# Performance work log

Hardware: AMD Instinct MI355X
Metric: run time of the kernel (lower is better)

## Reference

```python
import jax, jax.numpy as jnp
import numpy as np
import math

D = 768
H = 12
DFF = 3072
HD = D // H


def _layernorm(x, g, b, eps=1e-5):
    mu = jnp.mean(x, axis=-1, keepdims=True)
    var = jnp.var(x, axis=-1, keepdims=True)
    return (x - mu) * jax.lax.rsqrt(var + eps) * g + b


def setup_inputs() -> dict:
    key = jax.random.key(0)
    ks = jax.random.split(key, 12)
    B, S = 2, 4096
    s = 1.0 / math.sqrt(D)
    sf = 1.0 / math.sqrt(DFF)
    return {
        "x": jax.random.normal(ks[0], (B, S, D), jnp.float32),
        "attention_mask": jnp.ones((B, S), jnp.int32),
        "ln1_g": jnp.ones((D,), jnp.float32),
        "ln1_b": jnp.zeros((D,), jnp.float32),
        "ln2_g": jnp.ones((D,), jnp.float32),
        "ln2_b": jnp.zeros((D,), jnp.float32),
        "Wq": jax.random.normal(ks[1], (D, D), jnp.float32) * s,
        "bq": jnp.zeros((D,), jnp.float32),
        "Wk": jax.random.normal(ks[2], (D, D), jnp.float32) * s,
        "bk": jnp.zeros((D,), jnp.float32),
        "Wv": jax.random.normal(ks[3], (D, D), jnp.float32) * s,
        "bv": jnp.zeros((D,), jnp.float32),
        "Wo": jax.random.normal(ks[4], (D, D), jnp.float32) * s,
        "bo": jnp.zeros((D,), jnp.float32),
        "W1": jax.random.normal(ks[5], (D, DFF), jnp.float32) * s,
        "b1": jnp.zeros((DFF,), jnp.float32),
        "W2": jax.random.normal(ks[6], (DFF, D), jnp.float32) * sf,
        "b2": jnp.zeros((D,), jnp.float32),
    }


def _block(x, attention_mask, ln1_g, ln1_b, ln2_g, ln2_b,
           Wq, bq, Wk, bk, Wv, bv, Wo, bo, W1, b1, W2, b2):
    B, S, _ = x.shape
    h = _layernorm(x, ln1_g, ln1_b)
    q = (h @ Wq + bq).reshape(B, S, H, HD)
    k = (h @ Wk + bk).reshape(B, S, H, HD)
    v = (h @ Wv + bv).reshape(B, S, H, HD)
    # scores: [B, H, S, S]
    dots = jnp.einsum('bqhd,bkhd->bhqk', q, k) / math.sqrt(HD)
    causal = jnp.tril(jnp.ones((S, S), bool))  # True = keep
    keep = causal[None, None] & (attention_mask != 0)[:, None, None, :]
    dots = jnp.where(keep, dots, -jnp.inf)
    probs = jax.nn.softmax(dots, axis=-1)
    ctx = jnp.einsum('bhqk,bkhd->bqhd', probs, v).reshape(B, S, D)
    sa = ctx @ Wo + bo  # dropout = identity (eval)
    x = x + sa
    h2 = _layernorm(x, ln2_g, ln2_b)
    ff = jax.nn.relu(h2 @ W1 + b1) @ W2 + b2
    return x + ff


def reference(x, attention_mask, ln1_g, ln1_b, ln2_g, ln2_b,
              Wq, bq, Wk, bk, Wv, bv, Wo, bo, W1, b1, W2, b2):
    return _block(x, attention_mask, ln1_g, ln1_b, ln2_g, ln2_b,
                  Wq, bq, Wk, bk, Wv, bv, Wo, bo, W1, b1, W2, b2)
```

## Files before the change

kernel.cpp:

```cpp
#include <hip/hip_runtime.h>
#include <hip/hip_bf16.h>
#include <math.h>

#define S_LEN 4096
#define DMODEL 768
#define NHEAD 12
#define HDIM 64
#define DFF_ 3072
#define MROWS 8192

typedef __bf16 bf16;
typedef __bf16 bf16x4 __attribute__((ext_vector_type(4)));
typedef __bf16 bf16x8 __attribute__((ext_vector_type(8)));
typedef float f32x4 __attribute__((ext_vector_type(4)));
typedef short s16x4 __attribute__((ext_vector_type(4)));

union F4 { float4 v; float f[4]; };
union U2 { bf16 h[2]; unsigned u; };
union U8 { unsigned u[4]; bf16x8 v; };

#if __has_builtin(__builtin_amdgcn_mfma_f32_16x16x16bf16_1k)
typedef s16x4 mf16_t;
#define MFMA16(a, b, c) __builtin_amdgcn_mfma_f32_16x16x16bf16_1k((a), (b), (c), 0, 0, 0)
#define HAVE_MFMA16 1
#elif __has_builtin(__builtin_amdgcn_mfma_f32_16x16x16_bf16)
typedef bf16x4 mf16_t;
#define MFMA16(a, b, c) __builtin_amdgcn_mfma_f32_16x16x16_bf16((a), (b), (c), 0, 0, 0)
#define HAVE_MFMA16 1
#else
#define HAVE_MFMA16 0
#endif

#if HAVE_MFMA16
union U4 { unsigned u[2]; mf16_t v; };
#endif

__device__ __forceinline__ void gld_lds16(void* lds, const void* g) {
    __builtin_amdgcn_global_load_lds(
        (const __attribute__((address_space(1))) unsigned int*)g,
        (__attribute__((address_space(3))) unsigned int*)lds, 16, 0, 0);
}

template<typename OUT>
__global__ __launch_bounds__(256) void ln_kernel(const float* __restrict__ x,
                                                 const float* __restrict__ g,
                                                 const float* __restrict__ bta,
                                                 OUT* __restrict__ out,
                                                 float* __restrict__ zb) {
    const int row = blockIdx.x;
    const int t = threadIdx.x;
    if (zb && row == 0 && t < 192)
        ((float4*)zb)[t] = make_float4(0.f, 0.f, 0.f, 0.f);
    const float* xr = x + (size_t)row * DMODEL;
    float v0 = xr[t], v1 = xr[t + 256], v2 = xr[t + 512];
    float s = v0 + v1 + v2;
    float ss = v0 * v0 + v1 * v1 + v2 * v2;
    for (int o = 32; o > 0; o >>= 1) {
        s += __shfl_down(s, o, 64);
        ss += __shfl_down(ss, o, 64);
    }
    __shared__ float sm[4], sm2[4];
    const int w = t >> 6, lane = t & 63;
    if (lane == 0) { sm[w] = s; sm2[w] = ss; }
    __syncthreads();
    s = sm[0] + sm[1] + sm[2] + sm[3];
    ss = sm2[0] + sm2[1] + sm2[2] + sm2[3];
    const float mu = s * (1.0f / DMODEL);
    const float var = ss * (1.0f / DMODEL) - mu * mu;
    const float rs = rsqrtf(var + 1e-5f);
    OUT* orow = out + (size_t)row * DMODEL;
    orow[t]       = (OUT)((v0 - mu) * rs * g[t]       + bta[t]);
    orow[t + 256] = (OUT)((v1 - mu) * rs * g[t + 256] + bta[t + 256]);
    orow[t + 512] = (OUT)((v2 - mu) * rs * g[t + 512] + bta[t + 512]);
}

__global__ __launch_bounds__(256) void wtrans_all_kernel(
    const float* __restrict__ Wq, const float* __restrict__ Wk,
    const float* __restrict__ Wv, const float* __restrict__ Wo,
    const float* __restrict__ W1, const float* __restrict__ W2,
    bf16* __restrict__ Wqt, bf16* __restrict__ Wkt, bf16* __restrict__ Wvt,
    bf16* __restrict__ Wot, bf16* __restrict__ W1t, bf16* __restrict__ W2t) {
    int t = blockIdx.x;
    const float* W; bf16* Wt; int K, N;
    if      (t < 144)  { W = Wq; Wt = Wqt; K = 768;  N = 768;  }
    else if (t < 288)  { W = Wk; Wt = Wkt; K = 768;  N = 768;  t -= 144; }
    else if (t < 432)  { W = Wv; Wt = Wvt; K = 768;  N = 768;  t -= 288; }
    else if (t < 576)  { W = Wo; Wt = Wot; K = 768;  N = 768;  t -= 432; }
    else if (t < 1152) { W = W1; Wt = W1t; K = 768;  N = 3072; t -= 576; }
    else               { W = W2; Wt = W2t; K = 3072; N = 768;  t -= 1152; }
    const int nx = N >> 6;
    const int n0 = (t % nx) * 64, k0 = (t / nx) * 64;

    __shared__ float tile[64][65];
    const int tid = threadIdx.x;
    const int lr = tid >> 4, lc = (tid & 15) << 2;
#pragma unroll
    for (int i = 0; i < 4; ++i) {
        const int r = lr + i * 16;
        F4 w; w.v = *(const float4*)&W[(size_t)(k0 + r) * N + n0 + lc];
#pragma unroll
        for (int j = 0; j < 4; ++j) tile[r][lc + j] = w.f[j];
    }
    __syncthreads();
#pragma unroll
    for (int i = 0; i < 4; ++i) {
        const int n = lr + i * 16;
        bf16x4 o;
#pragma unroll
        for (int j = 0; j < 4; ++j) o[j] = (bf16)tile[lc + j][n];
        *(bf16x4*)&Wt[(size_t)(n0 + n) * K + k0 + lc] = o;
    }
}

template<int MT, bool RELU, bool RES, bool OUT_BF16>
__global__ __launch_bounds__(256) void mgemm_kernel(
    const bf16* __restrict__ A,
    const bf16* __restrict__ Wt0, const float* __restrict__ bias0, void* __restrict__ C0,
    const bf16* __restrict__ Wt1, const float* __restrict__ bias1, void* __restrict__ C1,
    const bf16* __restrict__ Wt2, const float* __restrict__ bias2, void* __restrict__ C2,
    const float* __restrict__ R, int M, int N, int K, int Kloop,
    int koff0, int koff1, int koff2,
    float sc0, float sc1, float sc2) {
    const bf16* Wt = Wt0; const float* bias = bias0; void* C = C0; float sc = sc0; int koff = koff0;
    if (blockIdx.z == 1) { Wt = Wt1; bias = bias1; C = C1; sc = sc1; koff = koff1; }
    if (blockIdx.z == 2) { Wt = Wt2; bias = bias2; C = C2; sc = sc2; koff = koff2; }

    constexpr int NI = (MT == 128) ? 4 : 2;
    __shared__ bf16 As[2][MT * 32];
    __shared__ bf16 Bs[2][128 * 32];

    const int tid = threadIdx.x;
    const int wave = tid >> 6, lane = tid & 63;
    const int row0 = blockIdx.y * MT, col0 = blockIdx.x * 128;
    const int wr = (MT == 128) ? (wave >> 1) * 64 : 0;
    const int wc = (MT == 128) ? (wave & 1) * 64 : wave * 32;
    const int mrow = lane & 15, kq = (lane >> 4) * 8;

    const int st_row = (lane >> 2);
    const int st_off = (lane & 3) * 16;

    f32x4 acc[4][NI] = {};

    const char* Ab = (const char*)(A + (size_t)row0 * K + koff);
    const char* Bb = (const char*)(Wt + (size_t)col0 * K + koff);
    const size_t strideA = (size_t)K * 2;

    for (int k0 = 0; k0 < Kloop; k0 += 64) {
#pragma unroll
        for (int s = 0; s < 2; ++s) {
            const int kk = k0 + s * 32;
            if (MT == 128) {
#pragma unroll
                for (int issue = 0; issue < 2; ++issue) {
                    const int r = wave * 32 + issue * 16 + st_row;
                    gld_lds16((char*)As[s] + (wave * 32 + issue * 16) * 64,
                              Ab + (size_t)r * strideA + kk * 2 + st_off);
                }
            } else {
                const int r = wave * 16 + st_row;
                gld_lds16((char*)As[s] + (wave * 16) * 64,
                          Ab + (size_t)r * strideA + kk * 2 + st_off);
            }
#pragma unroll
            for (int issue = 0; issue < 2; ++issue) {
                const int r = wave * 32 + issue * 16 + st_row;
                gld_lds16((char*)Bs[s] + (wave * 32 + issue * 16) * 64,
                          Bb + (size_t)r * strideA + kk * 2 + st_off);
            }
        }
        __syncthreads();
#pragma unroll
        for (int s = 0; s < 2; ++s) {
            bf16x8 af[4], bfr[NI];
#pragma unroll
            for (int mi = 0; mi < 4; ++mi)
                af[mi] = *(const bf16x8*)&As[s][(wr + mi * 16 + mrow) * 32 + kq];
#pragma unroll
            for (int ni = 0; ni < NI; ++ni)
                bfr[ni] = *(const bf16x8*)&Bs[s][(wc + ni * 16 + mrow) * 32 + kq];
#pragma unroll
            for (int mi = 0; mi < 4; ++mi)
#pragma unroll
                for (int ni = 0; ni < NI; ++ni)
                    acc[mi][ni] = __builtin_amdgcn_mfma_f32_16x16x32_bf16(
                        af[mi], bfr[ni], acc[mi][ni], 0, 0, 0);
        }
        __syncthreads();
    }

    const int quad = lane >> 4;
    float bv[NI];
#pragma unroll
    for (int ni = 0; ni < NI; ++ni) bv[ni] = bias[col0 + wc + ni * 16 + mrow];
#pragma unroll
    for (int mi = 0; mi < 4; ++mi) {
#pragma unroll
        for (int r = 0; r < 4; ++r) {
            const int row = row0 + wr + mi * 16 + quad * 4 + r;
#pragma unroll
            for (int ni = 0; ni < NI; ++ni) {
                const int col = col0 + wc + ni * 16 + mrow;
                float v = acc[mi][ni][r] + bv[ni];
                if (RES) v += R[(size_t)row * N + col];
                v *= sc;
                if (RELU) v = fmaxf(v, 0.0f);
                if (OUT_BF16) ((bf16*)C)[(size_t)row * N + col] = (bf16)v;
                else          ((float*)C)[(size_t)row * N + col] = v;
            }
        }
    }
}

__global__ __launch_bounds__(256) void ff2_combine_kernel(
    const bf16* __restrict__ p0, const bf16* __restrict__ p1,
    const float* __restrict__ b2, const float* __restrict__ x1,
    float* __restrict__ out) {
    const int i = (blockIdx.x * 256 + threadIdx.x) * 4;
    bf16x4 a = *(const bf16x4*)(p0 + i);
    bf16x4 b = *(const bf16x4*)(p1 + i);
    F4 xr; xr.v = *(const float4*)(x1 + i);
    const int col = i % DMODEL;
    F4 o;
#pragma unroll
    for (int j = 0; j < 4; ++j)
        o.f[j] = (float)a[j] + (float)b[j] + b2[col + j] + xr.f[j];
    *(float4*)(out + i) = o.v;
}

__global__ __launch_bounds__(256) void mattn_kernel(
    const bf16* __restrict__ Q, const bf16* __restrict__ K,
    const bf16* __restrict__ V, const int* __restrict__ amask,
    bf16* __restrict__ O) {
    const int qt = 63 - blockIdx.x;
    const int h = blockIdx.y, b = blockIdx.z;

    __shared__ bf16 Ks[2][64][68];
    __shared__ bf16 Vt[2][64][68];
    __shared__ float mk[2][64];
    __shared__ int flagv[2];

    const int tid = threadIdx.x;
    const int wave = tid >> 6, lane = tid & 63;
    const int l = lane & 15, quad = lane >> 4;
#if !HAVE_MFMA16
    const int qh = quad >> 1;
    const int srcA = (quad & 1) * 32 + l;
    const int srcB = srcA + 16;
#endif
    const float NEG_INF = -__builtin_huge_valf();

    const int kr = tid >> 2, ks = (tid & 3) * 16;
    const int vk0 = (tid & 31) * 2, vds = (tid >> 5) * 8;

    const bf16* Kbase = K + (size_t)b * S_LEN * DMODEL + h * HDIM;
    const bf16* Vbase = V + (size_t)b * S_LEN * DMODEL + h * HDIM;

#if HAVE_MFMA16
    U4 onesf;
    onesf.u[0] = 0x3F803F80u; onesf.u[1] = 0x3F803F80u;
#endif

    const bf16* Qb = Q + (size_t)(b * S_LEN + qt * 64 + wave * 16 + l) * DMODEL + h * HDIM;
    const bf16x8 qf0 = *(const bf16x8*)(Qb + quad * 8);
    const bf16x8 qf1 = *(const bf16x8*)(Qb + 32 + quad * 8);

    float m_run = NEG_INF;
#if !HAVE_MFMA16
    float l_run = 0.0f;
#endif
    f32x4 acc[4] = {};
#if HAVE_MFMA16
    f32x4 acc_l = {};
#endif

    bf16x8 kp0, kp1, vp0, vp1;
    int mv = 1;
    {
        const bf16* kg = Kbase + (size_t)kr * DMODEL + ks;
        kp0 = *(const bf16x8*)kg;
        kp1 = *(const bf16x8*)(kg + 8);
        const bf16* vg = Vbase + (size_t)vk0 * DMODEL + vds;
        vp0 = *(const bf16x8*)vg;
        vp1 = *(const bf16x8*)(vg + DMODEL);
        if (wave == 0) mv = amask[b * S_LEN + lane];
        *(bf16x8*)&Ks[0][kr][ks]     = kp0;
        *(bf16x8*)&Ks[0][kr][ks + 8] = kp1;
#pragma unroll
        for (int i = 0; i < 8; ++i) {
            U2 w; w.h[0] = vp0[i]; w.h[1] = vp1[i];
            *(unsigned*)&Vt[0][vds + i][vk0] = w.u;
        }
        if (wave == 0) {
            mk[0][lane] = mv ? 0.0f : NEG_INF;
            unsigned long long bal = __ballot(mv != 0);
            if (lane == 0) flagv[0] = (bal == ~0ULL);
        }
    }
    __syncthreads();
    int buf = 0;

    for (int kt = 0; kt <= qt; ++kt) {
        const bool more = (kt < qt);
        if (more) {
            const bf16* kg = Kbase + (size_t)((kt + 1) * 64 + kr) * DMODEL + ks;
            kp0 = *(const bf16x8*)kg;
            kp1 = *(const bf16x8*)(kg + 8);
            const bf16* vg = Vbase + (size_t)((kt + 1) * 64 + vk0) * DMODEL + vds;
            vp0 = *(const bf16x8*)vg;
            vp1 = *(const bf16x8*)(vg + DMODEL);
            if (wave == 0) mv = amask[b * S_LEN + (kt + 1) * 64 + lane];
        }

        const int allv = flagv[buf];
        f32x4 sreg[4] = {};
        __builtin_amdgcn_s_setprio(1);
#pragma unroll
        for (int mi = 0; mi < 4; ++mi) {
            bf16x8 kf0 = *(const bf16x8*)&Ks[buf][mi * 16 + l][quad * 8];
            bf16x8 kf1 = *(const bf16x8*)&Ks[buf][mi * 16 + l][32 + quad * 8];
            sreg[mi] = __builtin_amdgcn_mfma_f32_16x16x32_bf16(kf0, qf0, sreg[mi], 0, 0, 0);
            sreg[mi] = __builtin_amdgcn_mfma_f32_16x16x32_bf16(kf1, qf1, sreg[mi], 0, 0, 0);
        }
        __builtin_amdgcn_s_setprio(0);
        if (!allv) {
#pragma unroll
            for (int mi = 0; mi < 4; ++mi) {
                F4 m4; m4.v = *(const float4*)&mk[buf][mi * 16 + quad * 4];
#pragma unroll
                for (int r = 0; r < 4; ++r) sreg[mi][r] += m4.f[r];
            }
        }
        if (kt == qt) {
#pragma unroll
            for (int mi = 0; mi < 4; ++mi)
#pragma unroll
                for (int r = 0; r < 4; ++r)
                    if (mi * 16 + quad * 4 + r > wave * 16 + l)
                        sreg[mi][r] = NEG_INF;
        }

        float mloc = sreg[0][0];
#pragma unroll
        for (int mi = 0; mi < 4; ++mi)
#pragma unroll
            for (int r = 0; r < 4; ++r) mloc = fmaxf(mloc, sreg[mi][r]);
        mloc = fmaxf(mloc, __shfl_xor(mloc, 16, 64));
        mloc = fmaxf(mloc, __shfl_xor(mloc, 32, 64));
        if (__any(mloc > m_run + 8.0f)) {
            const float mn = fmaxf(m_run, mloc);
            const float alpha = __builtin_amdgcn_exp2f(m_run - mn);
            m_run = mn;
#pragma unroll
            for (int mi = 0; mi < 4; ++mi)
#pragma unroll
                for (int r = 0; r < 4; ++r) acc[mi][r] *= alpha;
#if HAVE_MFMA16
#pragma unroll
            for (int r = 0; r < 4; ++r) acc_l[r] *= alpha;
#else
            l_run *= alpha;
#endif
        }
#pragma unroll
        for (int mi = 0; mi < 4; ++mi)
#pragma unroll
            for (int r = 0; r < 4; ++r)
                sreg[mi][r] = __builtin_amdgcn_exp2f(sreg[mi][r] - m_run);
#if !HAVE_MFMA16
        float ls = 0.0f;
#pragma unroll
        for (int mi = 0; mi < 4; ++mi)
#pragma unroll
            for (int r = 0; r < 4; ++r) ls += sreg[mi][r];
        ls += __shfl_xor(ls, 16, 64);
        ls += __shfl_xor(ls, 32, 64);
        l_run += ls;
#endif

        unsigned pk[4][2];
#pragma unroll
        for (int mi = 0; mi < 4; ++mi) {
            U2 w0; w0.h[0] = (bf16)sreg[mi][0]; w0.h[1] = (bf16)sreg[mi][1];
            U2 w1; w1.h[0] = (bf16)sreg[mi][2]; w1.h[1] = (bf16)sreg[mi][3];
            pk[mi][0] = w0.u; pk[mi][1] = w1.u;
        }

#if HAVE_MFMA16
        __builtin_amdgcn_s_setprio(1);
#pragma unroll
        for (int mi = 0; mi < 4; ++mi) {
            U4 pb; pb.u[0] = pk[mi][0]; pb.u[1] = pk[mi][1];
#pragma unroll
            for (int di = 0; di < 4; ++di) {
                mf16_t va = *(const mf16_t*)&Vt[buf][di * 16 + l][mi * 16 + quad * 4];
                acc[di] = MFMA16(va, pb.v, acc[di]);
            }
            acc_l = MFMA16(onesf.v, pb.v, acc_l);
        }
        __builtin_amdgcn_s_setprio(0);
#else
        bf16x8 pfrag[2];
#pragma unroll
        for (int kc = 0; kc < 2; ++kc) {
            U8 u;
#pragma unroll
            for (int t = 0; t < 2; ++t) {
                const unsigned a0 = (unsigned)__shfl((int)pk[2 * kc][t],     srcA, 64);
                const unsigned b0 = (unsigned)__shfl((int)pk[2 * kc + 1][t], srcA, 64);
                u.u[t] = qh ? b0 : a0;
                const unsigned a1 = (unsigned)__shfl((int)pk[2 * kc][t],     srcB, 64);
                const unsigned b1 = (unsigned)__shfl((int)pk[2 * kc + 1][t], srcB, 64);
                u.u[2 + t] = qh ? b1 : a1;
            }
            pfrag[kc] = u.v;
        }
#pragma unroll
        for (int mi = 0; mi < 4; ++mi) {
            bf16x8 vf0 = *(const bf16x8*)&Vt[buf][mi * 16 + l][quad * 8];
            bf16x8 vf1 = *(const bf16x8*)&Vt[buf][mi * 16 + l][32 + quad * 8];
            acc[mi] = __builtin_amdgcn_mfma_f32_16x16x32_bf16(vf0, pfrag[0], acc[mi], 0, 0, 0);
            acc[mi] = __builtin_amdgcn_mfma_f32_16x16x32_bf16(vf1, pfrag[1], acc[mi], 0, 0, 0);
        }
#endif

        if (more) {
            const int nb = buf ^ 1;
            *(bf16x8*)&Ks[nb][kr][ks]     = kp0;
            *(bf16x8*)&Ks[nb][kr][ks + 8] = kp1;
#pragma unroll
            for (int i = 0; i < 8; ++i) {
                U2 w; w.h[0] = vp0[i]; w.h[1] = vp1[i];
                *(unsigned*)&Vt[nb][vds + i][vk0] = w.u;
            }
            if (wave == 0) {
                mk[nb][lane] = mv ? 0.0f : NEG_INF;
                unsigned long long bal = __ballot(mv != 0);
                if (lane == 0) flagv[nb] = (bal == ~0ULL);
            }
        }
        __syncthreads();
        buf ^= 1;
    }

#if HAVE_MFMA16
    const float l_fin = __shfl(acc_l[0], l, 64);
#else
    const float l_fin = l_run;
#endif
    const float rinv = 1.0f / l_fin;
    bf16 (*Os)[68] = (bf16 (*)[68])(&Ks[0][0][0]);
#pragma unroll
    for (int mi = 0; mi < 4; ++mi) {
        U2 w0; w0.h[0] = (bf16)(acc[mi][0] * rinv); w0.h[1] = (bf16)(acc[mi][1] * rinv);
        U2 w1; w1.h[0] = (bf16)(acc[mi][2] * rinv); w1.h[1] = (bf16)(acc[mi][3] * rinv);
        *(unsigned*)&Os[wave * 16 + l][mi * 16 + quad * 4]     = w0.u;
        *(unsigned*)&Os[wave * 16 + l][mi * 16 + quad * 4 + 2] = w1.u;
    }
    __syncthreads();
    {
        const int orow = tid >> 2, oseg = (tid & 3) * 16;
        bf16* Og = O + (size_t)(b * S_LEN + qt * 64 + orow) * DMODEL + h * HDIM + oseg;
        *(bf16x8*)Og       = *(const bf16x8*)&Os[orow][oseg];
        *(bf16x8*)(Og + 8) = *(const bf16x8*)&Os[orow][oseg + 8];
    }
}

extern "C" void kernel_launch(void* const* d_in, const int* in_sizes, int n_in,
                              void* d_out, int out_size, void* d_ws, size_t ws_size,
                              hipStream_t stream) {
    const float* x     = (const float*)d_in[0];
    const int*   amask = (const int*)  d_in[1];
    const float* ln1_g = (const float*)d_in[2];
    const float* ln1_b = (const float*)d_in[3];
    const float* ln2_g = (const float*)d_in[4];
    const float* ln2_b = (const float*)d_in[5];
    const float* Wq = (const float*)d_in[6];  const float* bq = (const float*)d_in[7];
    const float* Wk = (const float*)d_in[8];  const float* bk = (const float*)d_in[9];
    const float* Wv = (const float*)d_in[10]; const float* bv = (const float*)d_in[11];
    const float* Wo = (const float*)d_in[12]; const float* bo = (const float*)d_in[13];
    const float* W1 = (const float*)d_in[14]; const float* b1 = (const float*)d_in[15];
    const float* W2 = (const float*)d_in[16]; const float* b2 = (const float*)d_in[17];
    float* out = (float*)d_out;

    char* ws = (char*)d_ws;
    const size_t WSML = (size_t)DMODEL * DMODEL * 2;
    const size_t WBIG = (size_t)DMODEL * DFF_ * 2;
    bf16* Wqt = (bf16*)(ws + 0 * WSML);
    bf16* Wkt = (bf16*)(ws + 1 * WSML);
    bf16* Wvt = (bf16*)(ws + 2 * WSML);
    bf16* Wot = (bf16*)(ws + 3 * WSML);
    bf16* W1t = (bf16*)(ws + 4 * WSML);
    bf16* W2t = (bf16*)(ws + 4 * WSML + WBIG);
    char* act = ws + 4 * WSML + 2 * WBIG;

    const size_t HB = (size_t)MROWS * DMODEL * 2;
    const size_t FB = (size_t)MROWS * DMODEL * 4;
    bf16*  h    = (bf16*)(act);
    bf16*  qb   = (bf16*)(act + HB);
    bf16*  kb   = (bf16*)(act + 2 * HB);
    bf16*  vb   = (bf16*)(act + 3 * HB);
    bf16*  ctx  = h;
    float* x1   = (float*)(act + 4 * HB);
    bf16*  f    = (bf16*)(act + 4 * HB + FB);
    bf16*  h2   = h;
    bf16*  p0   = qb;
    bf16*  p1   = kb;
    float* zbias = (float*)vb;

    const float SCL = 0.125f * 1.44269504089f;

    wtrans_all_kernel<<<1728, 256, 0, stream>>>(Wq, Wk, Wv, Wo, W1, W2,
                                                Wqt, Wkt, Wvt, Wot, W1t, W2t);

    ln_kernel<bf16><<<MROWS, 256, 0, stream>>>(x, ln1_g, ln1_b, h, nullptr);
    mgemm_kernel<128, false, false, true><<<dim3(DMODEL / 128, MROWS / 128, 3), 256, 0, stream>>>(
        h, Wqt, bq, qb, Wkt, bk, kb, Wvt, bv, vb, nullptr,
        MROWS, DMODEL, DMODEL, DMODEL, 0, 0, 0, SCL, 1.0f, 1.0f);
    mattn_kernel<<<dim3(64, NHEAD, 2), 256, 0, stream>>>(qb, kb, vb, amask, ctx);
    mgemm_kernel<64, false, true, false><<<dim3(DMODEL / 128, MROWS / 64, 1), 256, 0, stream>>>(
        ctx, Wot, bo, x1, Wot, bo, x1, Wot, bo, x1, x,
        MROWS, DMODEL, DMODEL, DMODEL, 0, 0, 0, 1.0f, 1.0f, 1.0f);
    ln_kernel<bf16><<<MROWS, 256, 0, stream>>>(x1, ln2_g, ln2_b, h2, zbias);
    mgemm_kernel<128, true, false, true><<<dim3(DFF_ / 128, MROWS / 128, 1), 256, 0, stream>>>(
        h2, W1t, b1, f, W1t, b1, f, W1t, b1, f, nullptr,
        MROWS, DFF_, DMODEL, DMODEL, 0, 0, 0, 1.0f, 1.0f, 1.0f);
    mgemm_kernel<128, false, false, true><<<dim3(DMODEL / 128, MROWS / 128, 2), 256, 0, stream>>>(
        f, W2t, zbias, p0, W2t, zbias, p1, W2t, zbias, p1, nullptr,
        MROWS, DMODEL, DFF_, DFF_ / 2, 0, DFF_ / 2, 0, 1.0f, 1.0f, 1.0f);
    ff2_combine_kernel<<<(MROWS * DMODEL) / 1024, 256, 0, stream>>>(p0, p1, b2, x1, out);
}
```

Before: 518.5 us.

## Pair causal query tiles per block and load V via async LDS with transpose reads

The attention kernel now processes two query tiles per block (tile 63-bx and tile bx), so every block does the same amount of causal work, and the grid shrinks to half. V tiles are copied straight from global memory into LDS with global_load_lds, skipping the register round trip and the scalar transpose stores. The PV fragments are then read with ds_read_b64_tr_b16. The PV MFMA operands are swapped so the softmax rescale is applied per row through shuffles. This trades fewer, longer blocks (less occupancy and parallelism slack) for balanced load and a cheaper V staging path.

```diff
diff --git a/kernel.cpp b/kernel.cpp
--- a/kernel.cpp
+++ b/kernel.cpp
@@ -14,31 +14,31 @@
 typedef __bf16 bf16x8 __attribute__((ext_vector_type(8)));
 typedef float f32x4 __attribute__((ext_vector_type(4)));
 typedef short s16x4 __attribute__((ext_vector_type(4)));
+typedef s16x4 frag4;
 
 union F4 { float4 v; float f[4]; };
-union U2 { bf16 h[2]; unsigned u; };
-union U8 { unsigned u[4]; bf16x8 v; };
-
-#if __has_builtin(__builtin_amdgcn_mfma_f32_16x16x16bf16_1k)
-typedef s16x4 mf16_t;
-#define MFMA16(a, b, c) __builtin_amdgcn_mfma_f32_16x16x16bf16_1k((a), (b), (c), 0, 0, 0)
-#define HAVE_MFMA16 1
-#elif __has_builtin(__builtin_amdgcn_mfma_f32_16x16x16_bf16)
-typedef bf16x4 mf16_t;
-#define MFMA16(a, b, c) __builtin_amdgcn_mfma_f32_16x16x16_bf16((a), (b), (c), 0, 0, 0)
-#define HAVE_MFMA16 1
-#else
-#define HAVE_MFMA16 0
-#endif
-
-#if HAVE_MFMA16
-union U4 { unsigned u[2]; mf16_t v; };
-#endif
 
 __device__ __forceinline__ void gld_lds16(void* lds, const void* g) {
     __builtin_amdgcn_global_load_lds(
         (const __attribute__((address_space(1))) unsigned int*)g,
         (__attribute__((address_space(3))) unsigned int*)lds, 16, 0, 0);
+}
+
+__device__ __forceinline__ unsigned lds_off(const void* p) {
+    return (unsigned)(size_t)(const __attribute__((address_space(3))) char*)p;
+}
+
+__device__ __forceinline__ f32x4 mfma16(frag4 a, frag4 b, f32x4 c) {
+#if __has_builtin(__builtin_amdgcn_mfma_f32_16x16x16bf16_1k)
+    return __builtin_amdgcn_mfma_f32_16x16x16bf16_1k(a, b, c, 0, 0, 0);
+#else
+    union { frag4 s; bf16x4 h; } ua, ub; ua.s = a; ub.s = b;
+    bf16x8 a8 = {ua.h[0], ua.h[1], ua.h[2], ua.h[3],
+                 (bf16)0.f, (bf16)0.f, (bf16)0.f, (bf16)0.f};
+    bf16x8 b8 = {ub.h[0], ub.h[1], ub.h[2], ub.h[3],
+                 (bf16)0.f, (bf16)0.f, (bf16)0.f, (bf16)0.f};
+    return __builtin_amdgcn_mfma_f32_16x16x32_bf16(a8, b8, c, 0, 0, 0);
+#endif
 }
 
 template<typename OUT>
@@ -231,237 +231,201 @@
     const bf16* __restrict__ Q, const bf16* __restrict__ K,
     const bf16* __restrict__ V, const int* __restrict__ amask,
     bf16* __restrict__ O) {
-    const int qt = 63 - blockIdx.x;
-    const int h = blockIdx.y, b = blockIdx.z;
+    const int bx = blockIdx.x, h = blockIdx.y, b = blockIdx.z;
 
     __shared__ bf16 Ks[2][64][68];
-    __shared__ bf16 Vt[2][64][68];
+    __shared__ bf16 Vs[2][4096];
     __shared__ float mk[2][64];
     __shared__ int flagv[2];
 
     const int tid = threadIdx.x;
     const int wave = tid >> 6, lane = tid & 63;
     const int l = lane & 15, quad = lane >> 4;
-#if !HAVE_MFMA16
-    const int qh = quad >> 1;
-    const int srcA = (quad & 1) * 32 + l;
-    const int srcB = srcA + 16;
-#endif
     const float NEG_INF = -__builtin_huge_valf();
 
     const int kr = tid >> 2, ks = (tid & 3) * 16;
-    const int vk0 = (tid & 31) * 2, vds = (tid >> 5) * 8;
 
     const bf16* Kbase = K + (size_t)b * S_LEN * DMODEL + h * HDIM;
     const bf16* Vbase = V + (size_t)b * S_LEN * DMODEL + h * HDIM;
 
-#if HAVE_MFMA16
-    U4 onesf;
-    onesf.u[0] = 0x3F803F80u; onesf.u[1] = 0x3F803F80u;
-#endif
-
-    const bf16* Qb = Q + (size_t)(b * S_LEN + qt * 64 + wave * 16 + l) * DMODEL + h * HDIM;
-    const bf16x8 qf0 = *(const bf16x8*)(Qb + quad * 8);
-    const bf16x8 qf1 = *(const bf16x8*)(Qb + 32 + quad * 8);
-
-    float m_run = NEG_INF;
-#if !HAVE_MFMA16
-    float l_run = 0.0f;
-#endif
-    f32x4 acc[4] = {};
-#if HAVE_MFMA16
-    f32x4 acc_l = {};
-#endif
-
-    bf16x8 kp0, kp1, vp0, vp1;
-    int mv = 1;
+    int voff0, voff1;
     {
-        const bf16* kg = Kbase + (size_t)kr * DMODEL + ks;
-        kp0 = *(const bf16x8*)kg;
-        kp1 = *(const bf16x8*)(kg + 8);
-        const bf16* vg = Vbase + (size_t)vk0 * DMODEL + vds;
-        vp0 = *(const bf16x8*)vg;
-        vp1 = *(const bf16x8*)(vg + DMODEL);
-        if (wave == 0) mv = amask[b * S_LEN + lane];
-        *(bf16x8*)&Ks[0][kr][ks]     = kp0;
-        *(bf16x8*)&Ks[0][kr][ks + 8] = kp1;
-#pragma unroll
-        for (int i = 0; i < 8; ++i) {
-            U2 w; w.h[0] = vp0[i]; w.h[1] = vp1[i];
-            *(unsigned*)&Vt[0][vds + i][vk0] = w.u;
-        }
-        if (wave == 0) {
-            mk[0][lane] = mv ? 0.0f : NEG_INF;
-            unsigned long long bal = __ballot(mv != 0);
-            if (lane == 0) flagv[0] = (bal == ~0ULL);
-        }
-    }
-    __syncthreads();
-    int buf = 0;
-
-    for (int kt = 0; kt <= qt; ++kt) {
-        const bool more = (kt < qt);
-        if (more) {
-            const bf16* kg = Kbase + (size_t)((kt + 1) * 64 + kr) * DMODEL + ks;
+        const int g0 = tid, s0 = g0 >> 5;
+        voff0 = ((s0 >> 2) * 16 + ((g0 >> 1) & 15)) * DMODEL + (s0 & 3) * 16 + (g0 & 1) * 8;
+        const int g1 = 256 + tid, s1 = g1 >> 5;
+        voff1 = ((s1 >> 2) * 16 + ((g1 >> 1) & 15)) * DMODEL + (s1 & 3) * 16 + (g1 & 1) * 8;
+    }
+    const int vdst0 = (wave * 64) * 16;
+    const int vdst1 = (256 + wave * 64) * 16;
+
+    const frag4 onesf = {(short)0x3F80, (short)0x3F80, (short)0x3F80, (short)0x3F80};
+    const unsigned vtr0 = lds_off(&Vs[0][0]) + lane * 8;
+
+#pragma unroll 1
+    for (int pass = 0; pass < 2; ++pass) {
+        const int qt = pass ? bx : (63 - bx);
+
+        const bf16* Qb = Q + (size_t)(b * S_LEN + qt * 64 + wave * 16 + l) * DMODEL + h * HDIM;
+        const bf16x8 qf0 = *(const bf16x8*)(Qb + quad * 8);
+        const bf16x8 qf1 = *(const bf16x8*)(Qb + 32 + quad * 8);
+
+        float m_run = NEG_INF;
+        f32x4 acc[4] = {};
+        f32x4 acc_l = {};
+
+        bf16x8 kp0, kp1;
+        int mv = 1;
+        {
+            const bf16* kg = Kbase + (size_t)kr * DMODEL + ks;
             kp0 = *(const bf16x8*)kg;
             kp1 = *(const bf16x8*)(kg + 8);
-            const bf16* vg = Vbase + (size_t)((kt + 1) * 64 + vk0) * DMODEL + vds;
-            vp0 = *(const bf16x8*)vg;
-            vp1 = *(const bf16x8*)(vg + DMODEL);
-            if (wave == 0) mv = amask[b * S_LEN + (kt + 1) * 64 + lane];
-        }
-
-        const int allv = flagv[buf];
-        f32x4 sreg[4] = {};
-        __builtin_amdgcn_s_setprio(1);
-#pragma unroll
-        for (int mi = 0; mi < 4; ++mi) {
-            bf16x8 kf0 = *(const bf16x8*)&Ks[buf][mi * 16 + l][quad * 8];
-            bf16x8 kf1 = *(const bf16x8*)&Ks[buf][mi * 16 + l][32 + quad * 8];
-            sreg[mi] = __builtin_amdgcn_mfma_f32_16x16x32_bf16(kf0, qf0, sreg[mi], 0, 0, 0);
-            sreg[mi] = __builtin_amdgcn_mfma_f32_16x16x32_bf16(kf1, qf1, sreg[mi], 0, 0, 0);
-        }
-        __builtin_amdgcn_s_setprio(0);
-        if (!allv) {
+            gld_lds16((char*)Vs + vdst0, Vbase + voff0);
+            gld_lds16((char*)Vs + vdst1, Vbase + voff1);
+            if (wave == 0) mv = amask[b * S_LEN + lane];
+        }
+        __syncthreads();
+        {
+            *(bf16x8*)&Ks[0][kr][ks]     = kp0;
+            *(bf16x8*)&Ks[0][kr][ks + 8] = kp1;
+            if (wave == 0) {
+                mk[0][lane] = mv ? 0.0f : NEG_INF;
+                unsigned long long bal = __ballot(mv != 0);
+                if (lane == 0) flagv[0] = (bal == ~0ULL);
+            }
+        }
+        __syncthreads();
+        int buf = 0;
+
+        for (int kt = 0; kt <= qt; ++kt) {
+            const bool more = (kt < qt);
+            if (more) {
+                const bf16* kg = Kbase + (size_t)((kt + 1) * 64 + kr) * DMODEL + ks;
+                kp0 = *(const bf16x8*)kg;
+                kp1 = *(const bf16x8*)(kg + 8);
+                const bf16* vt = Vbase + (size_t)(kt + 1) * 64 * DMODEL;
+                const int nb = buf ^ 1;
+                gld_lds16((char*)Vs + nb * 8192 + vdst0, vt + voff0);
+                gld_lds16((char*)Vs + nb * 8192 + vdst1, vt + voff1);
+                if (wave == 0) mv = amask[b * S_LEN + (kt + 1) * 64 + lane];
+            }
+
+            const int allv = flagv[buf];
+            f32x4 sreg[4] = {};
+            __builtin_amdgcn_s_setprio(1);
 #pragma unroll
             for (int mi = 0; mi < 4; ++mi) {
-                F4 m4; m4.v = *(const float4*)&mk[buf][mi * 16 + quad * 4];
-#pragma unroll
-                for (int r = 0; r < 4; ++r) sreg[mi][r] += m4.f[r];
-            }
-        }
-        if (kt == qt) {
+                bf16x8 kf0 = *(const bf16x8*)&Ks[buf][mi * 16 + l][quad * 8];
+                bf16x8 kf1 = *(const bf16x8*)&Ks[buf][mi * 16 + l][32 + quad * 8];
+                sreg[mi] = __builtin_amdgcn_mfma_f32_16x16x32_bf16(kf0, qf0, sreg[mi], 0, 0, 0);
+                sreg[mi] = __builtin_amdgcn_mfma_f32_16x16x32_bf16(kf1, qf1, sreg[mi], 0, 0, 0);
+            }
+            __builtin_amdgcn_s_setprio(0);
+
+            frag4 va[16];
+            const unsigned vtr = vtr0 + buf * 8192;
+#define TRRD(i) asm volatile("ds_read_b64_tr_b16 %0, %1 offset:%2" \
+                             : "=v"(va[i]) : "v"(vtr), "i"((i) * 512))
+            TRRD(0);  TRRD(1);  TRRD(2);  TRRD(3);
+            TRRD(4);  TRRD(5);  TRRD(6);  TRRD(7);
+            TRRD(8);  TRRD(9);  TRRD(10); TRRD(11);
+            TRRD(12); TRRD(13); TRRD(14); TRRD(15);
+#undef TRRD
+
+            if (!allv) {
+#pragma unroll
+                for (int mi = 0; mi < 4; ++mi) {
+                    F4 m4; m4.v = *(const float4*)&mk[buf][mi * 16 + quad * 4];
+#pragma unroll
+                    for (int r = 0; r < 4; ++r) sreg[mi][r] += m4.f[r];
+                }
+            }
+            if (kt == qt) {
+#pragma unroll
+                for (int mi = 0; mi < 4; ++mi)
+#pragma unroll
+                    for (int r = 0; r < 4; ++r)
+                        if (mi * 16 + quad * 4 + r > wave * 16 + l)
+                            sreg[mi][r] = NEG_INF;
+            }
+
+            float mloc = sreg[0][0];
 #pragma unroll
             for (int mi = 0; mi < 4; ++mi)
 #pragma unroll
+                for (int r = 0; r < 4; ++r) mloc = fmaxf(mloc, sreg[mi][r]);
+            mloc = fmaxf(mloc, __shfl_xor(mloc, 16, 64));
+            mloc = fmaxf(mloc, __shfl_xor(mloc, 32, 64));
+            if (__any(mloc > m_run + 8.0f)) {
+                const float mn = fmaxf(m_run, mloc);
+                const float alpha = __builtin_amdgcn_exp2f(m_run - mn);
+                m_run = mn;
+                const float a0 = __shfl(alpha, quad * 4 + 0, 64);
+                const float a1 = __shfl(alpha, quad * 4 + 1, 64);
+                const float a2 = __shfl(alpha, quad * 4 + 2, 64);
+                const float a3 = __shfl(alpha, quad * 4 + 3, 64);
+#pragma unroll
+                for (int di = 0; di < 4; ++di) {
+                    acc[di][0] *= a0; acc[di][1] *= a1;
+                    acc[di][2] *= a2; acc[di][3] *= a3;
+                }
+                acc_l[0] *= a0; acc_l[1] *= a1; acc_l[2] *= a2; acc_l[3] *= a3;
+            }
+#pragma unroll
+            for (int mi = 0; mi < 4; ++mi)
+#pragma unroll
                 for (int r = 0; r < 4; ++r)
-                    if (mi * 16 + quad * 4 + r > wave * 16 + l)
-                        sreg[mi][r] = NEG_INF;
-        }
-
-        float mloc = sreg[0][0];
-#pragma unroll
-        for (int mi = 0; mi < 4; ++mi)
-#pragma unroll
-            for (int r = 0; r < 4; ++r) mloc = fmaxf(mloc, sreg[mi][r]);
-        mloc = fmaxf(mloc, __shfl_xor(mloc, 16, 64));
-        mloc = fmaxf(mloc, __shfl_xor(mloc, 32, 64));
-        if (__any(mloc > m_run + 8.0f)) {
-            const float mn = fmaxf(m_run, mloc);
-            const float alpha = __builtin_amdgcn_exp2f(m_run - mn);
-            m_run = mn;
-#pragma unroll
-            for (int mi = 0; mi < 4; ++mi)
-#pragma unroll
-                for (int r = 0; r < 4; ++r) acc[mi][r] *= alpha;
-#if HAVE_MFMA16
-#pragma unroll
-            for (int r = 0; r < 4; ++r) acc_l[r] *= alpha;
-#else
-            l_run *= alpha;
-#endif
-        }
-#pragma unroll
-        for (int mi = 0; mi < 4; ++mi)
-#pragma unroll
-            for (int r = 0; r < 4; ++r)
-                sreg[mi][r] = __builtin_amdgcn_exp2f(sreg[mi][r] - m_run);
-#if !HAVE_MFMA16
-        float ls = 0.0f;
-#pragma unroll
-        for (int mi = 0; mi < 4; ++mi)
-#pragma unroll
-            for (int r = 0; r < 4; ++r) ls += sreg[mi][r];
-        ls += __shfl_xor(ls, 16, 64);
-        ls += __shfl_xor(ls, 32, 64);
-        l_run += ls;
-#endif
-
-        unsigned pk[4][2];
-#pragma unroll
-        for (int mi = 0; mi < 4; ++mi) {
-            U2 w0; w0.h[0] = (bf16)sreg[mi][0]; w0.h[1] = (bf16)sreg[mi][1];
-            U2 w1; w1.h[0] = (bf16)sreg[mi][2]; w1.h[1] = (bf16)sreg[mi][3];
-            pk[mi][0] = w0.u; pk[mi][1] = w1.u;
-        }
-
-#if HAVE_MFMA16
-        __builtin_amdgcn_s_setprio(1);
-#pragma unroll
-        for (int mi = 0; mi < 4; ++mi) {
-            U4 pb; pb.u[0] = pk[mi][0]; pb.u[1] = pk[mi][1];
-#pragma unroll
-            for (int di = 0; di < 4; ++di) {
-                mf16_t va = *(const mf16_t*)&Vt[buf][di * 16 + l][mi * 16 + quad * 4];
-                acc[di] = MFMA16(va, pb.v, acc[di]);
-            }
-            acc_l = MFMA16(onesf.v, pb.v, acc_l);
-        }
-        __builtin_amdgcn_s_setprio(0);
-#else
-        bf16x8 pfrag[2];
-#pragma unroll
-        for (int kc = 0; kc < 2; ++kc) {
-            U8 u;
-#pragma unroll
-            for (int t = 0; t < 2; ++t) {
-                const unsigned a0 = (unsigned)__shfl((int)pk[2 * kc][t],     srcA, 64);
-                const unsigned b0 = (unsigned)__shfl((int)pk[2 * kc + 1][t], srcA, 64);
-                u.u[t] = qh ? b0 : a0;
-                const unsigned a1 = (unsigned)__shfl((int)pk[2 * kc][t],     srcB, 64);
-                const unsigned b1 = (unsigned)__shfl((int)pk[2 * kc + 1][t], srcB, 64);
-                u.u[2 + t] = qh ? b1 : a1;
-            }
-            pfrag[kc] = u.v;
-        }
-#pragma unroll
-        for (int mi = 0; mi < 4; ++mi) {
-            bf16x8 vf0 = *(const bf16x8*)&Vt[buf][mi * 16 + l][quad * 8];
-            bf16x8 vf1 = *(const bf16x8*)&Vt[buf][mi * 16 + l][32 + quad * 8];
-            acc[mi] = __builtin_amdgcn_mfma_f32_16x16x32_bf16(vf0, pfrag[0], acc[mi], 0, 0, 0);
-            acc[mi] = __builtin_amdgcn_mfma_f32_16x16x32_bf16(vf1, pfrag[1], acc[mi], 0, 0, 0);
-        }
-#endif
-
-        if (more) {
-            const int nb = buf ^ 1;
-            *(bf16x8*)&Ks[nb][kr][ks]     = kp0;
-            *(bf16x8*)&Ks[nb][kr][ks + 8] = kp1;
-#pragma unroll
-            for (int i = 0; i < 8; ++i) {
-                U2 w; w.h[0] = vp0[i]; w.h[1] = vp1[i];
-                *(unsigned*)&Vt[nb][vds + i][vk0] = w.u;
-            }
-            if (wave == 0) {
-                mk[nb][lane] = mv ? 0.0f : NEG_INF;
-                unsigned long long bal = __ballot(mv != 0);
-                if (lane == 0) flagv[nb] = (bal == ~0ULL);
-            }
+                    sreg[mi][r] = __builtin_amdgcn_exp2f(sreg[mi][r] - m_run);
+
+            frag4 pb[4];
+#pragma unroll
+            for (int mi = 0; mi < 4; ++mi) {
+                union { bf16x4 h; frag4 s; } u;
+                u.h[0] = (bf16)sreg[mi][0]; u.h[1] = (bf16)sreg[mi][1];
+                u.h[2] = (bf16)sreg[mi][2]; u.h[3] = (bf16)sreg[mi][3];
+                pb[mi] = u.s;
+            }
+
+            asm volatile("s_waitcnt lgkmcnt(0)" ::: "memory");
+            __builtin_amdgcn_sched_barrier(0);
+            __builtin_amdgcn_s_setprio(1);
+#pragma unroll
+            for (int mi = 0; mi < 4; ++mi) {
+#pragma unroll
+                for (int di = 0; di < 4; ++di)
+                    acc[di] = mfma16(pb[mi], va[mi * 4 + di], acc[di]);
+                acc_l = mfma16(pb[mi], onesf, acc_l);
+            }
+            __builtin_amdgcn_s_setprio(0);
+
+            if (more) {
+                const int nb = buf ^ 1;
+                *(bf16x8*)&Ks[nb][kr][ks]     = kp0;
+                *(bf16x8*)&Ks[nb][kr][ks + 8] = kp1;
+                if (wave == 0) {
+                    mk[nb][lane] = mv ? 0.0f : NEG_INF;
+                    unsigned long long bal = __ballot(mv != 0);
+                    if (lane == 0) flagv[nb] = (bal == ~0ULL);
+                }
+            }
+            __syncthreads();
+            buf ^= 1;
+        }
+
+        bf16 (*Os)[68] = (bf16 (*)[68])(&Ks[0][0][0]);
+#pragma unroll
+        for (int r = 0; r < 4; ++r) {
+            const float rinv = 1.0f / acc_l[r];
+#pragma unroll
+            for (int di = 0; di < 4; ++di)
+                Os[wave * 16 + quad * 4 + r][di * 16 + l] = (bf16)(acc[di][r] * rinv);
         }
         __syncthreads();
-        buf ^= 1;
-    }
-
-#if HAVE_MFMA16
-    const float l_fin = __shfl(acc_l[0], l, 64);
-#else
-    const float l_fin = l_run;
-#endif
-    const float rinv = 1.0f / l_fin;
-    bf16 (*Os)[68] = (bf16 (*)[68])(&Ks[0][0][0]);
-#pragma unroll
-    for (int mi = 0; mi < 4; ++mi) {
-        U2 w0; w0.h[0] = (bf16)(acc[mi][0] * rinv); w0.h[1] = (bf16)(acc[mi][1] * rinv);
-        U2 w1; w1.h[0] = (bf16)(acc[mi][2] * rinv); w1.h[1] = (bf16)(acc[mi][3] * rinv);
-        *(unsigned*)&Os[wave * 16 + l][mi * 16 + quad * 4]     = w0.u;
-        *(unsigned*)&Os[wave * 16 + l][mi * 16 + quad * 4 + 2] = w1.u;
-    }
-    __syncthreads();
-    {
-        const int orow = tid >> 2, oseg = (tid & 3) * 16;
-        bf16* Og = O + (size_t)(b * S_LEN + qt * 64 + orow) * DMODEL + h * HDIM + oseg;
-        *(bf16x8*)Og       = *(const bf16x8*)&Os[orow][oseg];
-        *(bf16x8*)(Og + 8) = *(const bf16x8*)&Os[orow][oseg + 8];
+        {
+            const int orow = tid >> 2, oseg = (tid & 3) * 16;
+            bf16* Og = O + (size_t)(b * S_LEN + qt * 64 + orow) * DMODEL + h * HDIM + oseg;
+            *(bf16x8*)Og       = *(const bf16x8*)&Os[orow][oseg];
+            *(bf16x8*)(Og + 8) = *(const bf16x8*)&Os[orow][oseg + 8];
+        }
     }
 }
 
@@ -516,7 +480,7 @@
     mgemm_kernel<128, false, false, true><<<dim3(DMODEL / 128, MROWS / 128, 3), 256, 0, stream>>>(
         h, Wqt, bq, qb, Wkt, bk, kb, Wvt, bv, vb, nullptr,
         MROWS, DMODEL, DMODEL, DMODEL, 0, 0, 0, SCL, 1.0f, 1.0f);
-    mattn_kernel<<<dim3(64, NHEAD, 2), 256, 0, stream>>>(qb, kb, vb, amask, ctx);
+    mattn_kernel<<<dim3(32, NHEAD, 2), 256, 0, stream>>>(qb, kb, vb, amask, ctx);
     mgemm_kernel<64, false, true, false><<<dim3(DMODEL / 128, MROWS / 64, 1), 256, 0, stream>>>(
         ctx, Wot, bo, x1, Wot, bo, x1, Wot, bo, x1, x,
         MROWS, DMODEL, DMODEL, DMODEL, 0, 0, 0, 1.0f, 1.0f, 1.0f);
```

Result: faster. 484.2 us (-6.6%).
